# Kernel tuning notes

Hardware: AMD Instinct MI355X
Metric: run time of the kernel (lower is better)

Reference implementation:

```python
import math
import jax, jax.numpy as jnp
import numpy as np

# Module hyperparameters (match init_kwargs)
EMBED = 512
H = 8            # n_heads
D = EMBED // H   # head_dim = 64
P = 32           # poly_dim
M = 4            # num_prf_features
R = 1            # num_quadrature_nodes
B = 1
T = 1024
EPS = 1e-6
C_CONST = 2.0 + EPS
# Gauss-Laguerre nodes/weights (R=1 -> node=1, weight=1), scaled by 1/C as in __init__
_nodes_np, _weights_np = np.polynomial.laguerre.laggauss(R)
QUAD_NODES = (_nodes_np / C_CONST).astype(np.float32)   # [R]


def setup_inputs() -> dict:
    key = jax.random.key(0)
    ks = jax.random.split(key, 6)
    x = jax.random.normal(ks[0], (B, T, EMBED), dtype=jnp.float32)
    qkv_w = jax.random.normal(ks[1], (3 * EMBED, EMBED), dtype=jnp.float32) * 0.02
    qkv_b = jnp.zeros((3 * EMBED,), dtype=jnp.float32)
    out_w = jax.random.normal(ks[2], (EMBED, EMBED), dtype=jnp.float32) * 0.02
    out_b = jnp.zeros((EMBED,), dtype=jnp.float32)
    omega = jax.random.normal(ks[3], (R, H, D, M), dtype=jnp.float32)  # PRF projection buffer
    poly_proj = jax.random.normal(ks[4], (H, D, P), dtype=jnp.float32) / math.sqrt(D)
    return {"x": x, "qkv_w": qkv_w, "qkv_b": qkv_b, "out_w": out_w,
            "out_b": out_b, "omega": omega, "poly_proj": poly_proj}


def _l2_normalize(z):
    # F.normalize(p=2, dim=-1), default eps=1e-12
    n = jnp.linalg.norm(z, axis=-1, keepdims=True)
    return z / jnp.maximum(n, 1e-12)


def _prf_features(x_norm, omega):
    # x_norm: [B,H,T,D], omega: [R,H,D,M] -> [R,B,H,T,M]
    proj = jnp.einsum('bhtd,rhdm->rbhtm', x_norm, omega)
    s = jnp.asarray(QUAD_NODES, x_norm.dtype).reshape(R, 1, 1, 1, 1)
    sqrt_2s = jnp.sqrt(2.0 * jnp.maximum(s, 0.0))
    exp_arg = jnp.clip(proj * sqrt_2s - s, -20.0, 20.0)
    return jnp.exp(exp_arg) / math.sqrt(M)


def _poly_features(x_norm, poly_proj):
    # squared random projection: [B,H,T,D] x [H,D,P] -> [B,H,T,P], nonneg
    p = jnp.einsum('bhtd,hdp->bhtp', x_norm, poly_proj)
    return p * p


def reference(x, qkv_w, qkv_b, out_w, out_b, omega, poly_proj):
    Bx, Tx, Cx = x.shape
    qkv = x @ qkv_w.T + qkv_b                       # [B,T,3C]
    q, k, v = jnp.split(qkv, 3, axis=-1)
    def to_heads(z):
        return z.reshape(Bx, Tx, H, D).transpose(0, 2, 1, 3)  # [B,H,T,D]
    q, k, v = to_heads(q), to_heads(k), to_heads(v)

    def full_features(z):
        zn = _l2_normalize(z)
        poly = _poly_features(zn, poly_proj)        # [B,H,T,P]
        prf = _prf_features(zn, omega)              # [R,B,H,T,M]
        return jnp.einsum('bhtp,rbhtm->rbhtpm', poly, prf)

    q_outer = full_features(q)                      # [R,B,H,T,P,M]
    k_outer = full_features(k)

    kv = jnp.einsum('rbhtpm,bhtd->rbhtpmd', k_outer, v)  # huge outer product
    kv_cumsum = jnp.cumsum(kv, axis=3)              # causal prefix sums along T
    k_cumsum = jnp.cumsum(k_outer, axis=3)

    context = jnp.einsum('rbhtpm,rbhtpmd->bhtd', q_outer, kv_cumsum)
    norm = jnp.einsum('rbhtpm,rbhtpm->bht', q_outer, k_cumsum)
    norm = jnp.maximum(norm, 1e-6)
    out = context / norm[..., None]                 # [B,H,T,D]

    out = out.transpose(0, 2, 1, 3).reshape(Bx, Tx, Cx)
    return out @ out_w.T + out_b
```

## Files before the change

kernel.cpp:

```cpp
#include <hip/hip_runtime.h>

#define T_LEN 1024
#define EMB   512
#define NH    8
#define HD    64
#define PDIM  32
#define MDIM  4
#define FDIM  128
#define TC    64
#define NC    16

typedef __attribute__((ext_vector_type(8))) short bf16x8;
typedef __attribute__((ext_vector_type(4))) float f32x4;

__device__ __forceinline__ unsigned short f2bf(float f) {
    unsigned u = __float_as_uint(f);
    unsigned r = u + 0x7fffu + ((u >> 16) & 1u);
    return (unsigned short)(r >> 16);
}
__device__ __forceinline__ float bf2f(unsigned short h) {
    return __uint_as_float(((unsigned)h) << 16);
}
__device__ __forceinline__ void split4(float4 v, ushort4& h4, ushort4& l4) {
    h4.x = f2bf(v.x); l4.x = f2bf(v.x - bf2f(h4.x));
    h4.y = f2bf(v.y); l4.y = f2bf(v.y - bf2f(h4.y));
    h4.z = f2bf(v.z); l4.z = f2bf(v.z - bf2f(h4.z));
    h4.w = f2bf(v.w); l4.w = f2bf(v.w - bf2f(h4.w));
}
__device__ __forceinline__ f32x4 mm3(bf16x8 ah, bf16x8 al, bf16x8 bh, bf16x8 bl, f32x4 acc) {
    acc = __builtin_amdgcn_mfma_f32_16x16x32_bf16(ah, bh, acc, 0, 0, 0);
    acc = __builtin_amdgcn_mfma_f32_16x16x32_bf16(ah, bl, acc, 0, 0, 0);
    acc = __builtin_amdgcn_mfma_f32_16x16x32_bf16(al, bh, acc, 0, 0, 0);
    return acc;
}
#define LD8(TILE, ROW, KB) (*reinterpret_cast<const bf16x8*>(&TILE[ROW][KB]))

__global__ __launch_bounds__(256) void k_qkv_mfma(
    const float* __restrict__ X, const float* __restrict__ W,
    const float* __restrict__ bias,
    const float* __restrict__ poly_proj, const float* __restrict__ omega,
    float* __restrict__ Vh,
    unsigned short* __restrict__ qfhi, unsigned short* __restrict__ qflo,
    unsigned short* __restrict__ kfhi, unsigned short* __restrict__ kflo)
{
    const int j0 = blockIdx.x * 64;
    const int t0 = blockIdx.y * 64;
    __shared__ __align__(16) unsigned short Ahi[64][80], Alo[64][80],
                                            Bhi[64][80], Blo[64][80];
    __shared__ float poly_s[64][33];
    __shared__ float prf_s[64][5];
    __shared__ float nrm2[2][64];
    const int tid = threadIdx.x, lane = tid & 63, wid = tid >> 6;
    const int wrow = (wid >> 1) * 32, wcol = (wid & 1) * 32;
    const int lr = lane & 15, lg = lane >> 4;
    f32x4 acc[2][2];
    #pragma unroll
    for (int i = 0; i < 2; ++i)
        #pragma unroll
        for (int j = 0; j < 2; ++j) acc[i][j] = (f32x4){0.f, 0.f, 0.f, 0.f};

    for (int k0 = 0; k0 < 512; k0 += 64) {
        #pragma unroll
        for (int l = 0; l < 4; ++l) {
            int ch = tid + l * 256;
            int row = ch >> 4, sg = (ch & 15) * 4;
            float4 av = *reinterpret_cast<const float4*>(&X[(size_t)(t0 + row) * 512 + k0 + sg]);
            ushort4 h4, l4; split4(av, h4, l4);
            *reinterpret_cast<ushort4*>(&Ahi[row][sg]) = h4;
            *reinterpret_cast<ushort4*>(&Alo[row][sg]) = l4;
            float4 bv = *reinterpret_cast<const float4*>(&W[(size_t)(j0 + row) * 512 + k0 + sg]);
            split4(bv, h4, l4);
            *reinterpret_cast<ushort4*>(&Bhi[row][sg]) = h4;
            *reinterpret_cast<ushort4*>(&Blo[row][sg]) = l4;
        }
        __syncthreads();
        #pragma unroll
        for (int kh = 0; kh < 2; ++kh) {
            const int kb = kh * 32 + lg * 8;
            bf16x8 ah0 = LD8(Ahi, wrow + lr, kb),      ah1 = LD8(Ahi, wrow + 16 + lr, kb);
            bf16x8 al0 = LD8(Alo, wrow + lr, kb),      al1 = LD8(Alo, wrow + 16 + lr, kb);
            bf16x8 bh0 = LD8(Bhi, wcol + lr, kb),      bh1 = LD8(Bhi, wcol + 16 + lr, kb);
            bf16x8 bl0 = LD8(Blo, wcol + lr, kb),      bl1 = LD8(Blo, wcol + 16 + lr, kb);
            acc[0][0] = mm3(ah0, al0, bh0, bl0, acc[0][0]);
            acc[0][1] = mm3(ah0, al0, bh1, bl1, acc[0][1]);
            acc[1][0] = mm3(ah1, al1, bh0, bl0, acc[1][0]);
            acc[1][1] = mm3(ah1, al1, bh1, bl1, acc[1][1]);
        }
        __syncthreads();
    }
    const int which = j0 >> 9;
    const int h = (j0 & 511) >> 6;

    if (which == 2) {
        #pragma unroll
        for (int i = 0; i < 2; ++i)
            #pragma unroll
            for (int j = 0; j < 2; ++j)
                #pragma unroll
                for (int r = 0; r < 4; ++r) {
                    int row = wrow + i * 16 + lg * 4 + r;
                    int col = wcol + j * 16 + lr;
                    Vh[(size_t)(h * T_LEN + t0 + row) * HD + col] = acc[i][j][r] + bias[j0 + col];
                }
        return;
    }

    #pragma unroll
    for (int i = 0; i < 2; ++i) {
        #pragma unroll
        for (int r = 0; r < 4; ++r) {
            int row = wrow + i * 16 + lg * 4 + r;
            float ss = 0.f;
            #pragma unroll
            for (int j = 0; j < 2; ++j) {
                int col = wcol + j * 16 + lr;
                float zv = acc[i][j][r] + bias[j0 + col];
                ss = fmaf(zv, zv, ss);
                unsigned short hv = f2bf(zv);
                Ahi[row][col] = hv;
                Alo[row][col] = f2bf(zv - bf2f(hv));
            }
            ss += __shfl_xor(ss, 1, 64);
            ss += __shfl_xor(ss, 2, 64);
            ss += __shfl_xor(ss, 4, 64);
            ss += __shfl_xor(ss, 8, 64);
            if (lr == 0) nrm2[wid & 1][row] = ss;
        }
    }
    {
        const float* P = poly_proj + (size_t)h * 64 * 32;
        int d = tid >> 2, p8 = (tid & 3) * 8;
        #pragma unroll
        for (int e = 0; e < 8; ++e) {
            float pv = P[d * 32 + p8 + e];
            unsigned short hv = f2bf(pv);
            Bhi[p8 + e][d] = hv;
            Blo[p8 + e][d] = f2bf(pv - bf2f(hv));
        }
        if (tid < 64) {
            const float* Om = omega + (size_t)h * 64 * 4;
            float4 om = *reinterpret_cast<const float4*>(&Om[tid * 4]);
            float oa[4] = {om.x, om.y, om.z, om.w};
            #pragma unroll
            for (int m = 0; m < 4; ++m) {
                unsigned short hv = f2bf(oa[m]);
                Bhi[32 + m][tid] = hv;
                Blo[32 + m][tid] = f2bf(oa[m] - bf2f(hv));
            }
        }
        for (int rr = tid; rr < 12 * 64; rr += 256) {
            int row = 36 + (rr >> 6), dd = rr & 63;
            Bhi[row][dd] = 0; Blo[row][dd] = 0;
        }
    }
    __syncthreads();
    const int mrow = wid * 16;
    f32x4 g[3];
    g[0] = g[1] = g[2] = (f32x4){0.f, 0.f, 0.f, 0.f};
    #pragma unroll
    for (int kh = 0; kh < 2; ++kh) {
        const int kb = kh * 32 + lg * 8;
        bf16x8 ah = LD8(Ahi, mrow + lr, kb), al = LD8(Alo, mrow + lr, kb);
        #pragma unroll
        for (int j = 0; j < 3; ++j) {
            bf16x8 bh = LD8(Bhi, j * 16 + lr, kb), bl = LD8(Blo, j * 16 + lr, kb);
            g[j] = mm3(ah, al, bh, bl, g[j]);
        }
    }
    const float S_NODE = (float)(1.0 / 2.000001);
    const float SQRT2S = sqrtf(2.0f * S_NODE);
    #pragma unroll
    for (int r = 0; r < 4; ++r) {
        int row = mrow + lg * 4 + r;
        float rn = 1.0f / fmaxf(sqrtf(nrm2[0][row] + nrm2[1][row]), 1e-12f);
        #pragma unroll
        for (int j = 0; j < 3; ++j) {
            float gv = g[j][r] * rn;
            if (j < 2) poly_s[row][j * 16 + lr] = gv * gv;
            else if (lr < 4) {
                float arg = fminf(fmaxf(fmaf(gv, SQRT2S, -S_NODE), -20.0f), 20.0f);
                prf_s[row][lr] = expf(arg) * 0.5f;
            }
        }
    }
    {
        int row = mrow + (lane >> 2), fq = lane & 3;
        float pr[8], pf[4];
        #pragma unroll
        for (int e = 0; e < 8; ++e) pr[e] = poly_s[row][fq * 8 + e];
        #pragma unroll
        for (int m = 0; m < 4; ++m) pf[m] = prf_s[row][m];
        int4 hi4[4], lo4[4];
        unsigned short* hp = reinterpret_cast<unsigned short*>(hi4);
        unsigned short* lp = reinterpret_cast<unsigned short*>(lo4);
        #pragma unroll
        for (int e = 0; e < 8; ++e)
            #pragma unroll
            for (int m = 0; m < 4; ++m) {
                float val = pr[e] * pf[m];
                unsigned short hv = f2bf(val);
                hp[e * 4 + m] = hv;
                lp[e * 4 + m] = f2bf(val - bf2f(hv));
            }
        unsigned short* dhi = (which == 0) ? qfhi : kfhi;
        unsigned short* dlo = (which == 0) ? qflo : kflo;
        size_t base = (size_t)(h * T_LEN + t0 + row) * FDIM + fq * 32;
        #pragma unroll
        for (int s = 0; s < 4; ++s) {
            *reinterpret_cast<int4*>(&dhi[base + s * 8]) = hi4[s];
            *reinterpret_cast<int4*>(&dlo[base + s * 8]) = lo4[s];
        }
    }
}

__global__ __launch_bounds__(256) void k_out_mfma(
    const unsigned short* __restrict__ AThi, const unsigned short* __restrict__ ATlo,
    const float* __restrict__ W, const float* __restrict__ bias,
    float* __restrict__ Y)
{
    const int j0 = blockIdx.x * 64;
    const int t0 = blockIdx.y * 64;
    __shared__ __align__(16) unsigned short Ahi[64][80], Alo[64][80],
                                            Bhi[64][80], Blo[64][80];
    const int tid = threadIdx.x, lane = tid & 63, wid = tid >> 6;
    const int wrow = (wid >> 1) * 32, wcol = (wid & 1) * 32;
    const int lr = lane & 15, lg = lane >> 4;
    f32x4 acc[2][2];
    #pragma unroll
    for (int i = 0; i < 2; ++i)
        #pragma unroll
        for (int j = 0; j < 2; ++j) acc[i][j] = (f32x4){0.f, 0.f, 0.f, 0.f};

    for (int k0 = 0; k0 < 512; k0 += 64) {
        #pragma unroll
        for (int l = 0; l < 2; ++l) {
            int ch = tid + l * 256;
            int row = ch >> 3, sg = (ch & 7) * 8;
            size_t ao = (size_t)(t0 + row) * 512 + k0 + sg;
            *reinterpret_cast<int4*>(&Ahi[row][sg]) = *reinterpret_cast<const int4*>(&AThi[ao]);
            *reinterpret_cast<int4*>(&Alo[row][sg]) = *reinterpret_cast<const int4*>(&ATlo[ao]);
        }
        #pragma unroll
        for (int l = 0; l < 4; ++l) {
            int ch = tid + l * 256;
            int row = ch >> 4, sg = (ch & 15) * 4;
            float4 bv = *reinterpret_cast<const float4*>(&W[(size_t)(j0 + row) * 512 + k0 + sg]);
            ushort4 h4, l4; split4(bv, h4, l4);
            *reinterpret_cast<ushort4*>(&Bhi[row][sg]) = h4;
            *reinterpret_cast<ushort4*>(&Blo[row][sg]) = l4;
        }
        __syncthreads();
        #pragma unroll
        for (int kh = 0; kh < 2; ++kh) {
            const int kb = kh * 32 + lg * 8;
            bf16x8 ah0 = LD8(Ahi, wrow + lr, kb),      ah1 = LD8(Ahi, wrow + 16 + lr, kb);
            bf16x8 al0 = LD8(Alo, wrow + lr, kb),      al1 = LD8(Alo, wrow + 16 + lr, kb);
            bf16x8 bh0 = LD8(Bhi, wcol + lr, kb),      bh1 = LD8(Bhi, wcol + 16 + lr, kb);
            bf16x8 bl0 = LD8(Blo, wcol + lr, kb),      bl1 = LD8(Blo, wcol + 16 + lr, kb);
            acc[0][0] = mm3(ah0, al0, bh0, bl0, acc[0][0]);
            acc[0][1] = mm3(ah0, al0, bh1, bl1, acc[0][1]);
            acc[1][0] = mm3(ah1, al1, bh0, bl0, acc[1][0]);
            acc[1][1] = mm3(ah1, al1, bh1, bl1, acc[1][1]);
        }
        __syncthreads();
    }
    #pragma unroll
    for (int i = 0; i < 2; ++i)
        #pragma unroll
        for (int j = 0; j < 2; ++j)
            #pragma unroll
            for (int r = 0; r < 4; ++r) {
                int row = wrow + i * 16 + lg * 4 + r;
                int col = wcol + j * 16 + lr;
                Y[(size_t)(t0 + row) * EMB + j0 + col] = acc[i][j][r] + bias[j0 + col];
            }
}

__global__ __launch_bounds__(256) void k_chunk_kv(
    const unsigned short* __restrict__ kfhi, const unsigned short* __restrict__ kflo,
    const float* __restrict__ Vh,
    float* __restrict__ Sch, float* __restrict__ zch)
{
    const int b = blockIdx.x;
    const int fh = b & 1, hc = b >> 1, h = hc >> 4, c = hc & 15;
    const int t0 = c * TC;
    const int tid = threadIdx.x, lane = tid & 63, wid = tid >> 6;
    const int wrow = (wid >> 1) * 32, wcol = (wid & 1) * 32;
    const int lr = lane & 15, lg = lane >> 4;
    __shared__ __align__(16) unsigned short Ahi[64][80], Alo[64][80],
                                            Bhi[64][80], Blo[64][80];
    #pragma unroll
    for (int l = 0; l < 2; ++l) {
        int ch = tid + l * 256;
        int t = ch >> 3, f8 = (ch & 7) * 8;
        int tb = t >> 3, tl = t & 7, m = f8 >> 3;
        size_t ko = (size_t)((h << 10) + t0 + t) * FDIM + fh * 64 + f8;
        int4 hv = *reinterpret_cast<const int4*>(&kfhi[ko]);
        int4 lv = *reinterpret_cast<const int4*>(&kflo[ko]);
        const unsigned short* hp = reinterpret_cast<const unsigned short*>(&hv);
        const unsigned short* lp = reinterpret_cast<const unsigned short*>(&lv);
        int col = ((tb ^ m) << 3) + tl;
        #pragma unroll
        for (int j = 0; j < 8; ++j) {
            Ahi[f8 + j][col] = hp[j];
            Alo[f8 + j][col] = lp[j];
        }
    }
    #pragma unroll
    for (int l = 0; l < 4; ++l) {
        int ch = tid + l * 256;
        int t = ch >> 4, d4 = (ch & 15) * 4;
        int tb = t >> 3, tl = t & 7;
        float4 vv = *reinterpret_cast<const float4*>(&Vh[(size_t)((h << 10) + t0 + t) * HD + d4]);
        float arr[4] = {vv.x, vv.y, vv.z, vv.w};
        #pragma unroll
        for (int j = 0; j < 4; ++j) {
            int row = d4 + j;
            int col = ((tb ^ ((row >> 3) & 7)) << 3) + tl;
            unsigned short hv2 = f2bf(arr[j]);
            Bhi[row][col] = hv2;
            Blo[row][col] = f2bf(arr[j] - bf2f(hv2));
        }
    }
    __syncthreads();
    f32x4 acc[2][2];
    #pragma unroll
    for (int i = 0; i < 2; ++i)
        #pragma unroll
        for (int j = 0; j < 2; ++j) acc[i][j] = (f32x4){0.f, 0.f, 0.f, 0.f};
    #pragma unroll
    for (int kh = 0; kh < 2; ++kh) {
        const int kb = kh * 32 + lg * 8, cb = kb >> 3;
        const int d0 = wcol + lr, d1 = wcol + 16 + lr;
        const int c0 = ((cb ^ ((d0 >> 3) & 7)) << 3), c1 = ((cb ^ ((d1 >> 3) & 7)) << 3);
        bf16x8 bh0 = *reinterpret_cast<const bf16x8*>(&Bhi[d0][c0]);
        bf16x8 bl0 = *reinterpret_cast<const bf16x8*>(&Blo[d0][c0]);
        bf16x8 bh1 = *reinterpret_cast<const bf16x8*>(&Bhi[d1][c1]);
        bf16x8 bl1 = *reinterpret_cast<const bf16x8*>(&Blo[d1][c1]);
        #pragma unroll
        for (int fi = 0; fi < 2; ++fi) {
            int fr = wrow + fi * 16 + lr;
            int ca = ((cb ^ ((fr >> 3) & 7)) << 3);
            bf16x8 ah = *reinterpret_cast<const bf16x8*>(&Ahi[fr][ca]);
            bf16x8 al = *reinterpret_cast<const bf16x8*>(&Alo[fr][ca]);
            acc[fi][0] = mm3(ah, al, bh0, bl0, acc[fi][0]);
            acc[fi][1] = mm3(ah, al, bh1, bl1, acc[fi][1]);
        }
    }
    if (tid < 64) {
        float s = 0.f;
        const int g = (tid >> 3) & 7;
        #pragma unroll
        for (int cb2 = 0; cb2 < 8; ++cb2) {
            int base = ((cb2 ^ g) << 3);
            #pragma unroll
            for (int e = 0; e < 8; ++e)
                s += bf2f(Ahi[tid][base + e]) + bf2f(Alo[tid][base + e]);
        }
        zch[(h * NC + c) * FDIM + fh * 64 + tid] = s;
    }
    float* S = Sch + (size_t)(h * NC + c) * FDIM * HD;
    #pragma unroll
    for (int fi = 0; fi < 2; ++fi)
        #pragma unroll
        for (int dj = 0; dj < 2; ++dj)
            #pragma unroll
            for (int r = 0; r < 4; ++r) {
                int f = fh * 64 + wrow + fi * 16 + lg * 4 + r;
                int d = wcol + dj * 16 + lr;
                S[f * HD + d] = acc[fi][dj][r];
            }
}

__global__ __launch_bounds__(256) void k_attn_mfma(
    const unsigned short* __restrict__ qfhi, const unsigned short* __restrict__ qflo,
    const unsigned short* __restrict__ kfhi, const unsigned short* __restrict__ kflo,
    const float* __restrict__ Sch, const float* __restrict__ Vh,
    const float* __restrict__ zch,
    unsigned short* __restrict__ AThi, unsigned short* __restrict__ ATlo)
{
    const int b = blockIdx.x;
    const int h = b >> 5, c = (b >> 1) & 15, half = b & 1;
    const int tc0 = c * TC;
    const int tq0 = tc0 + half * 32;
    const int tid = threadIdx.x, lane = tid & 63, wid = tid >> 6;
    const int wrow = (wid >> 1) * 16, wcol = (wid & 1) * 32;
    const int lr = lane & 15, lg = lane >> 4;

    __shared__ __align__(16) unsigned short T0[32][80], T1[32][80];
    __shared__ __align__(16) unsigned short T2[64][80], T3[64][80];
    __shared__ __align__(16) unsigned short T4[64][80], T5[64][80];
    __shared__ unsigned short zhi[FDIM], zlo[FDIM];
    __shared__ float nrm_part[2][32], nrm[32];

    if (tid < FDIM) {
        float zv = 0.f;
        for (int cc = 0; cc < c; ++cc) zv += zch[(h * NC + cc) * FDIM + tid];
        unsigned short zh = f2bf(zv);
        zhi[tid] = zh; zlo[tid] = f2bf(zv - bf2f(zh));
    }

    f32x4 accA[2], accC[2], accN;
    accA[0] = accA[1] = accC[0] = accC[1] = accN = (f32x4){0.f, 0.f, 0.f, 0.f};

    for (int f0 = 0; f0 < FDIM; f0 += 64) {
        {
            int row = tid >> 3, sg = (tid & 7) * 8;
            size_t qo = (size_t)(h * T_LEN + tq0 + row) * FDIM + f0 + sg;
            *reinterpret_cast<int4*>(&T0[row][sg]) = *reinterpret_cast<const int4*>(&qfhi[qo]);
            *reinterpret_cast<int4*>(&T1[row][sg]) = *reinterpret_cast<const int4*>(&qflo[qo]);
        }
        #pragma unroll
        for (int l = 0; l < 2; ++l) {
            int ch = tid + l * 256;
            int row = ch >> 3, sg = (ch & 7) * 8;
            size_t ko = (size_t)(h * T_LEN + tc0 + row) * FDIM + f0 + sg;
            *reinterpret_cast<int4*>(&T2[row][sg]) = *reinterpret_cast<const int4*>(&kfhi[ko]);
            *reinterpret_cast<int4*>(&T3[row][sg]) = *reinterpret_cast<const int4*>(&kflo[ko]);
        }
        #pragma unroll
        for (int l = 0; l < 4; ++l) {
            int ch = tid + l * 256;
            int f = ch >> 4, d4 = (ch & 15) * 4;
            int fb = f >> 3, fl = f & 7;
            float4 sv = make_float4(0.f, 0.f, 0.f, 0.f);
            for (int cc = 0; cc < c; ++cc) {
                float4 t = *reinterpret_cast<const float4*>(
                    &Sch[((size_t)((h * NC + cc) * FDIM + f0 + f)) * HD + d4]);
                sv.x += t.x; sv.y += t.y; sv.z += t.z; sv.w += t.w;
            }
            float arr[4] = {sv.x, sv.y, sv.z, sv.w};
            #pragma unroll
            for (int j = 0; j < 4; ++j) {
                int row = d4 + j;
                int col = ((fb ^ ((row >> 3) & 7)) << 3) + fl;
                unsigned short hv = f2bf(arr[j]);
                T4[row][col] = hv;
                T5[row][col] = f2bf(arr[j] - bf2f(hv));
            }
        }
        __syncthreads();
        #pragma unroll
        for (int kh = 0; kh < 2; ++kh) {
            const int kb = kh * 32 + lg * 8, cb = kb >> 3;
            bf16x8 qh = LD8(T0, wrow + lr, kb), ql = LD8(T1, wrow + lr, kb);
            bf16x8 kh0 = LD8(T2, wcol + lr, kb),      kh1 = LD8(T2, wcol + 16 + lr, kb);
            bf16x8 kl0 = LD8(T3, wcol + lr, kb),      kl1 = LD8(T3, wcol + 16 + lr, kb);
            const int d0 = wcol + lr, d1 = wcol + 16 + lr;
            const int c0 = ((cb ^ ((d0 >> 3) & 7)) << 3), c1 = ((cb ^ ((d1 >> 3) & 7)) << 3);
            bf16x8 sh0 = *reinterpret_cast<const bf16x8*>(&T4[d0][c0]);
            bf16x8 sl0 = *reinterpret_cast<const bf16x8*>(&T5[d0][c0]);
            bf16x8 sh1 = *reinterpret_cast<const bf16x8*>(&T4[d1][c1]);
            bf16x8 sl1 = *reinterpret_cast<const bf16x8*>(&T5[d1][c1]);
            accA[0] = mm3(qh, ql, kh0, kl0, accA[0]);
            accA[1] = mm3(qh, ql, kh1, kl1, accA[1]);
            accC[0] = mm3(qh, ql, sh0, sl0, accC[0]);
            accC[1] = mm3(qh, ql, sh1, sl1, accC[1]);
            bf16x8 zh8, zl8;
            #pragma unroll
            for (int j = 0; j < 8; ++j) {
                zh8[j] = (short)zhi[f0 + kb + j];
                zl8[j] = (short)zlo[f0 + kb + j];
            }
            accN = mm3(qh, ql, zh8, zl8, accN);
        }
        __syncthreads();
    }

    #pragma unroll
    for (int r = 0; r < 4; ++r) {
        int rowl = wrow + lg * 4 + r;
        int rowc = half * 32 + rowl;
        float rs = 0.f;
        #pragma unroll
        for (int j = 0; j < 2; ++j) {
            int col = wcol + j * 16 + lr;
            float vA = (col <= rowc) ? accA[j][r] : 0.f;
            rs += vA;
            unsigned short hv = f2bf(vA);
            T0[rowl][col] = hv;
            T1[rowl][col] = f2bf(vA - bf2f(hv));
        }
        #pragma unroll
        for (int off = 1; off < 16; off <<= 1) rs += __shfl_xor(rs, off, 64);
        if (lr == 0) {
            if ((wid & 1) == 0) nrm_part[0][rowl] = rs + accN[r];
            else                nrm_part[1][rowl] = rs;
        }
    }
    #pragma unroll
    for (int l = 0; l < 4; ++l) {
        int ch = tid + l * 256;
        int t = ch >> 4, d4 = (ch & 15) * 4;
        int tb = t >> 3, tl = t & 7;
        float4 vv = *reinterpret_cast<const float4*>(&Vh[(size_t)(h * T_LEN + tc0 + t) * HD + d4]);
        float arr[4] = {vv.x, vv.y, vv.z, vv.w};
        #pragma unroll
        for (int j = 0; j < 4; ++j) {
            int row = d4 + j;
            int col = ((tb ^ ((row >> 3) & 7)) << 3) + tl;
            unsigned short hv = f2bf(arr[j]);
            T2[row][col] = hv;
            T3[row][col] = f2bf(arr[j] - bf2f(hv));
        }
    }
    __syncthreads();
    if (tid < 32) nrm[tid] = fmaxf(nrm_part[0][tid] + nrm_part[1][tid], 1e-6f);

    #pragma unroll
    for (int kh = 0; kh < 2; ++kh) {
        const int kb = kh * 32 + lg * 8, cb = kb >> 3;
        bf16x8 ah = LD8(T0, wrow + lr, kb), al = LD8(T1, wrow + lr, kb);
        const int d0 = wcol + lr, d1 = wcol + 16 + lr;
        const int c0 = ((cb ^ ((d0 >> 3) & 7)) << 3), c1 = ((cb ^ ((d1 >> 3) & 7)) << 3);
        bf16x8 vh0 = *reinterpret_cast<const bf16x8*>(&T2[d0][c0]);
        bf16x8 vl0 = *reinterpret_cast<const bf16x8*>(&T3[d0][c0]);
        bf16x8 vh1 = *reinterpret_cast<const bf16x8*>(&T2[d1][c1]);
        bf16x8 vl1 = *reinterpret_cast<const bf16x8*>(&T3[d1][c1]);
        accC[0] = mm3(ah, al, vh0, vl0, accC[0]);
        accC[1] = mm3(ah, al, vh1, vl1, accC[1]);
    }
    __syncthreads();

    #pragma unroll
    for (int j = 0; j < 2; ++j)
        #pragma unroll
        for (int r = 0; r < 4; ++r) {
            int rowl = wrow + lg * 4 + r;
            int col = wcol + j * 16 + lr;
            float o = accC[j][r] / nrm[rowl];
            unsigned short hv = f2bf(o);
            size_t oi = (size_t)(tq0 + rowl) * EMB + h * HD + col;
            AThi[oi] = hv; ATlo[oi] = f2bf(o - bf2f(hv));
        }
}

extern "C" void kernel_launch(void* const* d_in, const int* in_sizes, int n_in,
                              void* d_out, int out_size, void* d_ws, size_t ws_size,
                              hipStream_t stream) {
    const float* x         = (const float*)d_in[0];
    const float* qkv_w     = (const float*)d_in[1];
    const float* qkv_b     = (const float*)d_in[2];
    const float* out_w     = (const float*)d_in[3];
    const float* out_b     = (const float*)d_in[4];
    const float* omega     = (const float*)d_in[5];
    const float* poly_proj = (const float*)d_in[6];
    float* out = (float*)d_out;

    float* ws = (float*)d_ws;
    float* v = ws;
    unsigned short* qfhi = (unsigned short*)(v + 524288);
    unsigned short* qflo = qfhi + 1048576;
    unsigned short* kfhi = qflo + 1048576;
    unsigned short* kflo = kfhi + 1048576;
    float* Sch  = (float*)(kflo + 1048576);
    float* zch  = Sch + 1048576;
    unsigned short* AThi = (unsigned short*)(zch + 16384);
    unsigned short* ATlo = AThi + 524288;

    k_qkv_mfma<<<dim3(24, 16), 256, 0, stream>>>(x, qkv_w, qkv_b, poly_proj, omega,
                                                 v, qfhi, qflo, kfhi, kflo);
    k_chunk_kv<<<256, 256, 0, stream>>>(kfhi, kflo, v, Sch, zch);
    k_attn_mfma<<<NH * NC * 2, 256, 0, stream>>>(qfhi, qflo, kfhi, kflo,
                                                 Sch, v, zch, AThi, ATlo);
    k_out_mfma<<<dim3(8, 16), 256, 0, stream>>>(AThi, ATlo, out_w, out_b, out);
}
```

Before: 135.5 us.

## Pre-split inputs to bf16 hi/lo planes, store V split, add chunk prefix-sum kernel

A new conversion kernel splits X, the QKV weight and the output weight into bf16 hi/lo planes once, so the GEMM tiles load them directly instead of re-splitting every tile in every block. V is now stored already split, so the chunk and attention kernels load it with 16-byte reads. A separate prefix kernel computes exclusive prefix sums of the chunk KV states and normalizers, replacing the per-block serial loop over earlier chunks in the attention kernel. The cost is two extra kernel launches and the extra global traffic of writing and reading the split copies.

```diff
diff --git a/kernel.cpp b/kernel.cpp
--- a/kernel.cpp
+++ b/kernel.cpp
@@ -35,11 +35,30 @@
 }
 #define LD8(TILE, ROW, KB) (*reinterpret_cast<const bf16x8*>(&TILE[ROW][KB]))
 
+__global__ __launch_bounds__(256) void k_cvt(
+    const float* __restrict__ X, const float* __restrict__ Wq,
+    const float* __restrict__ Wo,
+    unsigned short* __restrict__ Xhi, unsigned short* __restrict__ Xlo,
+    unsigned short* __restrict__ Whi, unsigned short* __restrict__ Wlo,
+    unsigned short* __restrict__ Ohi, unsigned short* __restrict__ Olo)
+{
+    int i = (blockIdx.x * 256 + threadIdx.x) * 4;
+    const float* src; unsigned short *dh, *dl; int off;
+    if (i < 524288)       { src = X;  dh = Xhi; dl = Xlo; off = i; }
+    else if (i < 1310720) { src = Wq; dh = Whi; dl = Wlo; off = i - 524288; }
+    else                  { src = Wo; dh = Ohi; dl = Olo; off = i - 1310720; }
+    float4 v = *reinterpret_cast<const float4*>(&src[off]);
+    ushort4 h4, l4; split4(v, h4, l4);
+    *reinterpret_cast<ushort4*>(&dh[off]) = h4;
+    *reinterpret_cast<ushort4*>(&dl[off]) = l4;
+}
+
 __global__ __launch_bounds__(256) void k_qkv_mfma(
-    const float* __restrict__ X, const float* __restrict__ W,
+    const unsigned short* __restrict__ Xhi, const unsigned short* __restrict__ Xlo,
+    const unsigned short* __restrict__ Whi, const unsigned short* __restrict__ Wlo,
     const float* __restrict__ bias,
     const float* __restrict__ poly_proj, const float* __restrict__ omega,
-    float* __restrict__ Vh,
+    unsigned short* __restrict__ Vhi, unsigned short* __restrict__ Vlo,
     unsigned short* __restrict__ qfhi, unsigned short* __restrict__ qflo,
     unsigned short* __restrict__ kfhi, unsigned short* __restrict__ kflo)
 {
@@ -61,17 +80,15 @@
 
     for (int k0 = 0; k0 < 512; k0 += 64) {
         #pragma unroll
-        for (int l = 0; l < 4; ++l) {
+        for (int l = 0; l < 2; ++l) {
             int ch = tid + l * 256;
-            int row = ch >> 4, sg = (ch & 15) * 4;
-            float4 av = *reinterpret_cast<const float4*>(&X[(size_t)(t0 + row) * 512 + k0 + sg]);
-            ushort4 h4, l4; split4(av, h4, l4);
-            *reinterpret_cast<ushort4*>(&Ahi[row][sg]) = h4;
-            *reinterpret_cast<ushort4*>(&Alo[row][sg]) = l4;
-            float4 bv = *reinterpret_cast<const float4*>(&W[(size_t)(j0 + row) * 512 + k0 + sg]);
-            split4(bv, h4, l4);
-            *reinterpret_cast<ushort4*>(&Bhi[row][sg]) = h4;
-            *reinterpret_cast<ushort4*>(&Blo[row][sg]) = l4;
+            int row = ch >> 3, sg = (ch & 7) * 8;
+            size_t ao = (size_t)(t0 + row) * 512 + k0 + sg;
+            size_t bo = (size_t)(j0 + row) * 512 + k0 + sg;
+            *reinterpret_cast<int4*>(&Ahi[row][sg]) = *reinterpret_cast<const int4*>(&Xhi[ao]);
+            *reinterpret_cast<int4*>(&Alo[row][sg]) = *reinterpret_cast<const int4*>(&Xlo[ao]);
+            *reinterpret_cast<int4*>(&Bhi[row][sg]) = *reinterpret_cast<const int4*>(&Whi[bo]);
+            *reinterpret_cast<int4*>(&Blo[row][sg]) = *reinterpret_cast<const int4*>(&Wlo[bo]);
         }
         __syncthreads();
         #pragma unroll
@@ -100,7 +117,10 @@
                 for (int r = 0; r < 4; ++r) {
                     int row = wrow + i * 16 + lg * 4 + r;
                     int col = wcol + j * 16 + lr;
-                    Vh[(size_t)(h * T_LEN + t0 + row) * HD + col] = acc[i][j][r] + bias[j0 + col];
+                    float val = acc[i][j][r] + bias[j0 + col];
+                    unsigned short hv = f2bf(val);
+                    size_t vi = (size_t)(h * T_LEN + t0 + row) * HD + col;
+                    Vhi[vi] = hv; Vlo[vi] = f2bf(val - bf2f(hv));
                 }
         return;
     }
@@ -215,8 +235,8 @@
 
 __global__ __launch_bounds__(256) void k_out_mfma(
     const unsigned short* __restrict__ AThi, const unsigned short* __restrict__ ATlo,
-    const float* __restrict__ W, const float* __restrict__ bias,
-    float* __restrict__ Y)
+    const unsigned short* __restrict__ Ohi, const unsigned short* __restrict__ Olo,
+    const float* __restrict__ bias, float* __restrict__ Y)
 {
     const int j0 = blockIdx.x * 64;
     const int t0 = blockIdx.y * 64;
@@ -237,17 +257,11 @@
             int ch = tid + l * 256;
             int row = ch >> 3, sg = (ch & 7) * 8;
             size_t ao = (size_t)(t0 + row) * 512 + k0 + sg;
+            size_t bo = (size_t)(j0 + row) * 512 + k0 + sg;
             *reinterpret_cast<int4*>(&Ahi[row][sg]) = *reinterpret_cast<const int4*>(&AThi[ao]);
             *reinterpret_cast<int4*>(&Alo[row][sg]) = *reinterpret_cast<const int4*>(&ATlo[ao]);
-        }
-        #pragma unroll
-        for (int l = 0; l < 4; ++l) {
-            int ch = tid + l * 256;
-            int row = ch >> 4, sg = (ch & 15) * 4;
-            float4 bv = *reinterpret_cast<const float4*>(&W[(size_t)(j0 + row) * 512 + k0 + sg]);
-            ushort4 h4, l4; split4(bv, h4, l4);
-            *reinterpret_cast<ushort4*>(&Bhi[row][sg]) = h4;
-            *reinterpret_cast<ushort4*>(&Blo[row][sg]) = l4;
+            *reinterpret_cast<int4*>(&Bhi[row][sg]) = *reinterpret_cast<const int4*>(&Ohi[bo]);
+            *reinterpret_cast<int4*>(&Blo[row][sg]) = *reinterpret_cast<const int4*>(&Olo[bo]);
         }
         __syncthreads();
         #pragma unroll
@@ -278,7 +292,7 @@
 
 __global__ __launch_bounds__(256) void k_chunk_kv(
     const unsigned short* __restrict__ kfhi, const unsigned short* __restrict__ kflo,
-    const float* __restrict__ Vh,
+    const unsigned short* __restrict__ Vhi, const unsigned short* __restrict__ Vlo,
     float* __restrict__ Sch, float* __restrict__ zch)
 {
     const int b = blockIdx.x;
@@ -309,18 +323,16 @@
     #pragma unroll
     for (int l = 0; l < 4; ++l) {
         int ch = tid + l * 256;
-        int t = ch >> 4, d4 = (ch & 15) * 4;
+        int plane = ch >> 9, rem = ch & 511;
+        int t = rem >> 3, d8 = (rem & 7) * 8;
         int tb = t >> 3, tl = t & 7;
-        float4 vv = *reinterpret_cast<const float4*>(&Vh[(size_t)((h << 10) + t0 + t) * HD + d4]);
-        float arr[4] = {vv.x, vv.y, vv.z, vv.w};
-        #pragma unroll
-        for (int j = 0; j < 4; ++j) {
-            int row = d4 + j;
-            int col = ((tb ^ ((row >> 3) & 7)) << 3) + tl;
-            unsigned short hv2 = f2bf(arr[j]);
-            Bhi[row][col] = hv2;
-            Blo[row][col] = f2bf(arr[j] - bf2f(hv2));
-        }
+        const unsigned short* src = plane ? Vlo : Vhi;
+        int4 vv = *reinterpret_cast<const int4*>(&src[(size_t)((h << 10) + t0 + t) * HD + d8]);
+        const unsigned short* vp = reinterpret_cast<const unsigned short*>(&vv);
+        int col = ((tb ^ (d8 >> 3)) << 3) + tl;
+        unsigned short (*dst)[80] = plane ? Blo : Bhi;
+        #pragma unroll
+        for (int j = 0; j < 8; ++j) dst[d8 + j][col] = vp[j];
     }
     __syncthreads();
     f32x4 acc[2][2];
@@ -372,11 +384,39 @@
             }
 }
 
+__global__ __launch_bounds__(256) void k_prefix(
+    const float* __restrict__ Sch, const float* __restrict__ zch,
+    float* __restrict__ Spre, float* __restrict__ zpre)
+{
+    const int h = blockIdx.x >> 5;
+    const int e = ((blockIdx.x & 31) << 8) + threadIdx.x;
+    const size_t base = (size_t)h * NC * FDIM * HD + e;
+    float vals[NC];
+    #pragma unroll
+    for (int c = 0; c < NC; ++c) vals[c] = Sch[base + (size_t)c * FDIM * HD];
+    float run = 0.0f;
+    #pragma unroll
+    for (int c = 0; c < NC; ++c) {
+        Spre[base + (size_t)c * FDIM * HD] = run;
+        run += vals[c];
+    }
+    if ((blockIdx.x & 31) == 0 && threadIdx.x < FDIM) {
+        const int zb = h * NC * FDIM + threadIdx.x;
+        float zv[NC];
+        #pragma unroll
+        for (int c = 0; c < NC; ++c) zv[c] = zch[zb + c * FDIM];
+        float zr = 0.0f;
+        #pragma unroll
+        for (int c = 0; c < NC; ++c) { zpre[zb + c * FDIM] = zr; zr += zv[c]; }
+    }
+}
+
 __global__ __launch_bounds__(256) void k_attn_mfma(
     const unsigned short* __restrict__ qfhi, const unsigned short* __restrict__ qflo,
     const unsigned short* __restrict__ kfhi, const unsigned short* __restrict__ kflo,
-    const float* __restrict__ Sch, const float* __restrict__ Vh,
-    const float* __restrict__ zch,
+    const float* __restrict__ Spre,
+    const unsigned short* __restrict__ Vhi, const unsigned short* __restrict__ Vlo,
+    const float* __restrict__ zpre,
     unsigned short* __restrict__ AThi, unsigned short* __restrict__ ATlo)
 {
     const int b = blockIdx.x;
@@ -394,8 +434,7 @@
     __shared__ float nrm_part[2][32], nrm[32];
 
     if (tid < FDIM) {
-        float zv = 0.f;
-        for (int cc = 0; cc < c; ++cc) zv += zch[(h * NC + cc) * FDIM + tid];
+        float zv = zpre[(h * NC + c) * FDIM + tid];
         unsigned short zh = f2bf(zv);
         zhi[tid] = zh; zlo[tid] = f2bf(zv - bf2f(zh));
     }
@@ -423,12 +462,8 @@
             int ch = tid + l * 256;
             int f = ch >> 4, d4 = (ch & 15) * 4;
             int fb = f >> 3, fl = f & 7;
-            float4 sv = make_float4(0.f, 0.f, 0.f, 0.f);
-            for (int cc = 0; cc < c; ++cc) {
-                float4 t = *reinterpret_cast<const float4*>(
-                    &Sch[((size_t)((h * NC + cc) * FDIM + f0 + f)) * HD + d4]);
-                sv.x += t.x; sv.y += t.y; sv.z += t.z; sv.w += t.w;
-            }
+            float4 sv = *reinterpret_cast<const float4*>(
+                &Spre[((size_t)((h * NC + c) * FDIM + f0 + f)) * HD + d4]);
             float arr[4] = {sv.x, sv.y, sv.z, sv.w};
             #pragma unroll
             for (int j = 0; j < 4; ++j) {
@@ -491,18 +526,16 @@
     #pragma unroll
     for (int l = 0; l < 4; ++l) {
         int ch = tid + l * 256;
-        int t = ch >> 4, d4 = (ch & 15) * 4;
+        int plane = ch >> 9, rem = ch & 511;
+        int t = rem >> 3, d8 = (rem & 7) * 8;
         int tb = t >> 3, tl = t & 7;
-        float4 vv = *reinterpret_cast<const float4*>(&Vh[(size_t)(h * T_LEN + tc0 + t) * HD + d4]);
-        float arr[4] = {vv.x, vv.y, vv.z, vv.w};
-        #pragma unroll
-        for (int j = 0; j < 4; ++j) {
-            int row = d4 + j;
-            int col = ((tb ^ ((row >> 3) & 7)) << 3) + tl;
-            unsigned short hv = f2bf(arr[j]);
-            T2[row][col] = hv;
-            T3[row][col] = f2bf(arr[j] - bf2f(hv));
-        }
+        const unsigned short* src = plane ? Vlo : Vhi;
+        int4 vv = *reinterpret_cast<const int4*>(&src[(size_t)(h * T_LEN + tc0 + t) * HD + d8]);
+        const unsigned short* vp = reinterpret_cast<const unsigned short*>(&vv);
+        int col = ((tb ^ (d8 >> 3)) << 3) + tl;
+        unsigned short (*dst)[80] = plane ? T3 : T2;
+        #pragma unroll
+        for (int j = 0; j < 8; ++j) dst[d8 + j][col] = vp[j];
     }
     __syncthreads();
     if (tid < 32) nrm[tid] = fmaxf(nrm_part[0][tid] + nrm_part[1][tid], 1e-6f);
@@ -547,21 +580,32 @@
     const float* poly_proj = (const float*)d_in[6];
     float* out = (float*)d_out;
 
-    float* ws = (float*)d_ws;
-    float* v = ws;
-    unsigned short* qfhi = (unsigned short*)(v + 524288);
+    unsigned short* Xhi  = (unsigned short*)d_ws;
+    unsigned short* Xlo  = Xhi + 524288;
+    unsigned short* Whi  = Xlo + 524288;
+    unsigned short* Wlo  = Whi + 786432;
+    unsigned short* Ohi  = Wlo + 786432;
+    unsigned short* Olo  = Ohi + 262144;
+    unsigned short* Vhi  = Olo + 262144;
+    unsigned short* Vlo  = Vhi + 524288;
+    unsigned short* qfhi = Vlo + 524288;
     unsigned short* qflo = qfhi + 1048576;
     unsigned short* kfhi = qflo + 1048576;
     unsigned short* kflo = kfhi + 1048576;
     float* Sch  = (float*)(kflo + 1048576);
-    float* zch  = Sch + 1048576;
-    unsigned short* AThi = (unsigned short*)(zch + 16384);
-    unsigned short* ATlo = AThi + 524288;
-
-    k_qkv_mfma<<<dim3(24, 16), 256, 0, stream>>>(x, qkv_w, qkv_b, poly_proj, omega,
-                                                 v, qfhi, qflo, kfhi, kflo);
-    k_chunk_kv<<<256, 256, 0, stream>>>(kfhi, kflo, v, Sch, zch);
-    k_attn_mfma<<<NH * NC * 2, 256, 0, stream>>>(qfhi, qflo, kfhi, kflo,
-                                                 Sch, v, zch, AThi, ATlo);
-    k_out_mfma<<<dim3(8, 16), 256, 0, stream>>>(AThi, ATlo, out_w, out_b, out);
-}
+    float* Spre = Sch + 1048576;
+    float* zch  = Spre + 1048576;
+    float* zpre = zch + 16384;
+    unsigned short* AThi = Xhi;
+    unsigned short* ATlo = Xlo;
+
+    k_cvt<<<1536, 256, 0, stream>>>(x, qkv_w, out_w, Xhi, Xlo, Whi, Wlo, Ohi, Olo);
+    k_qkv_mfma<<<dim3(24, 16), 256, 0, stream>>>(Xhi, Xlo, Whi, Wlo, qkv_b,
+                                                 poly_proj, omega, Vhi, Vlo,
+                                                 qfhi, qflo, kfhi, kflo);
+    k_chunk_kv<<<256, 256, 0, stream>>>(kfhi, kflo, Vhi, Vlo, Sch, zch);
+    k_prefix<<<256, 256, 0, stream>>>(Sch, zch, Spre, zpre);
+    k_attn_mfma<<<NH * NC * 2, 256, 0, stream>>>(qfhi, qflo, kfhi, kflo, Spre,
+                                                 Vhi, Vlo, zpre, AThi, ATlo);
+    k_out_mfma<<<dim3(8, 16), 256, 0, stream>>>(AThi, ATlo, Ohi, Olo, out_b, out);
+}
```

After: 112.2 us. 17.3% less time.
